# Kernel tuning notes

Measured on AMD Instinct MI355X. Metric: run time of the kernel, lower is better.

## Reference

```python
import jax, jax.numpy as jnp
import numpy as np

FEAT, HW, C, M, U, B = 2048, 14, 20, 64, 128, 4


def _grid_sample_one(img, grid):
    # img: [M, H, W]; grid: [H, W, 2] normalized coords (x, y), align_corners=True, zero padding
    H, W = img.shape[-2], img.shape[-1]
    gx = (grid[..., 0] + 1.0) * 0.5 * (W - 1)
    gy = (grid[..., 1] + 1.0) * 0.5 * (H - 1)
    x0 = jnp.floor(gx).astype(jnp.int32); x1 = x0 + 1
    y0 = jnp.floor(gy).astype(jnp.int32); y1 = y0 + 1

    def gather(yi, xi):
        valid = (yi >= 0) & (yi < H) & (xi >= 0) & (xi < W)
        yc = jnp.clip(yi, 0, H - 1); xc = jnp.clip(xi, 0, W - 1)
        return img[:, yc, xc] * valid.astype(img.dtype)  # [M, H, W]

    w00 = (x1 - gx) * (y1 - gy); w01 = (gx - x0) * (y1 - gy)
    w10 = (x1 - gx) * (gy - y0); w11 = (gx - x0) * (gy - y0)
    return (gather(y0, x0) * w00 + gather(y0, x1) * w01 +
            gather(y1, x0) * w10 + gather(y1, x1) * w11)


def setup_inputs() -> dict:
    key = jax.random.key(0)
    ks = jax.random.split(key, 5)
    x = jax.random.normal(ks[0], (B, FEAT, HW, HW), jnp.float32)
    W_parcel = jax.random.normal(ks[1], (C, M, FEAT), jnp.float32) * 0.02
    W_stn = jax.random.normal(ks[2], (C, 6, M * (HW // 2) ** 2), jnp.float32) * 1e-3
    b_stn = jnp.tile(jnp.array([1.0, 0.0, 0.0, 0.0, 1.0, 0.0], jnp.float32), (C, 1))
    Wg = jax.random.normal(ks[3], (C, C - 1, U, 2 * M), jnp.float32) * 0.02
    w_phi = jax.random.normal(ks[4], (1, U), jnp.float32) * 0.05
    b_phi = jnp.zeros((1,), jnp.float32)
    return {"x": x, "W_parcel": W_parcel, "W_stn": W_stn, "b_stn": b_stn,
            "Wg": Wg, "w_phi": w_phi, "b_phi": b_phi}


def reference(x, W_parcel, W_stn, b_stn, Wg, w_phi, b_phi):
    b, _, H, W = x.shape
    # per-class 1x1 conv parcels: [B, C, M, H, W]
    x_tmp = jnp.einsum('bfhw,cmf->bcmhw', x, W_parcel)
    # relu + 2x2 maxpool -> [B, C, M, 7, 7]
    pooled = jax.nn.relu(x_tmp).reshape(b, C, M, H // 2, 2, W // 2, 2).max(axis=(4, 6))
    flat = pooled.reshape(b, C, M * (H // 2) * (W // 2))
    theta = (jnp.einsum('bck,cjk->bcj', flat, W_stn) + b_stn).reshape(b, C, 2, 3)
    # affine grid (align_corners=True): base[h, w] = [x_norm, y_norm, 1]
    xs = jnp.linspace(-1.0, 1.0, W); ys = jnp.linspace(-1.0, 1.0, H)
    base = jnp.stack(jnp.broadcast_arrays(xs[None, :], ys[:, None], jnp.ones((H, W))), -1)
    grid = jnp.einsum('bcij,hwj->bchwi', theta, base)  # [B, C, H, W, 2]
    # STN sampling of the pre-relu parcel maps
    x_obj = jax.vmap(jax.vmap(_grid_sample_one))(x_tmp, grid)  # [B, C, M, H, W]
    # pairwise relation: relu(Wa[i,j] x_obj[i] + Wb[i,j] x_obj[j]) summed over j != i
    jidx = jnp.asarray(np.array([[k for k in range(C) if k != c] for c in range(C)]))
    Wa, Wb = Wg[..., :M], Wg[..., M:]
    A = jnp.einsum('ckum,bcmhw->bckuhw', Wa, x_obj)
    Bp = jnp.einsum('ckum,bckmhw->bckuhw', Wb, x_obj[:, jidx])
    rel = jax.nn.relu(A + Bp).sum(axis=2)          # [B, C, U, H, W]
    rel_mean = rel.mean(axis=(-2, -1))             # [B, C, U]  (adaptive avg pool 1x1)
    out = jnp.einsum('bcu,ou->bco', rel_mean, w_phi)[..., 0] + b_phi  # [B, C]
    return out
```

## Files before the change

### kernel.cpp

```cpp
#include <hip/hip_runtime.h>

#define FEAT 2048
#define HWD 14
#define NPIX 196
#define C_CLS 20
#define M_DIM 64
#define U_DIM 128
#define B_SZ 4
#define K_REL 19
#define NPOOL 49

typedef __attribute__((ext_vector_type(8))) short bf16x8s;
typedef __attribute__((ext_vector_type(8))) unsigned short ushort8v;
typedef __attribute__((ext_vector_type(4))) float f32x4;
typedef __attribute__((ext_vector_type(4))) unsigned int uint4v;

__device__ inline unsigned short f2bf(float f) {
    unsigned u = __builtin_bit_cast(unsigned, f);
    unsigned r = (u + 0x7FFF + ((u >> 16) & 1)) >> 16;
    return (unsigned short)r;
}

__device__ inline bf16x8s cvt8(const float* __restrict__ p) {
    float4 lo = *(const float4*)p;
    float4 hi = *(const float4*)(p + 4);
    bf16x8s r;
    r[0] = (short)f2bf(lo.x); r[1] = (short)f2bf(lo.y);
    r[2] = (short)f2bf(lo.z); r[3] = (short)f2bf(lo.w);
    r[4] = (short)f2bf(hi.x); r[5] = (short)f2bf(hi.y);
    r[6] = (short)f2bf(hi.z); r[7] = (short)f2bf(hi.w);
    return r;
}

__global__ __launch_bounds__(256) void prep_kernel(
        const float* __restrict__ x, const float* __restrict__ Wg,
        const float* __restrict__ Wp,
        unsigned short* __restrict__ xts, unsigned short* __restrict__ Wgb,
        unsigned short* __restrict__ Awp) {
    __shared__ unsigned short T[64][210];
    const int blk = blockIdx.x;
    const int tid = threadIdx.x;
    if (blk < 128) {
        const int b = blk >> 5;
        const int s = blk & 31;
        const float* xb = x + ((size_t)b * FEAT + s * 64) * NPIX;
        for (int i = tid; i < 64 * NPIX; i += 256) {
            int kk = i / NPIX, hw = i - kk * NPIX;
            T[kk][hw] = f2bf(xb[(size_t)kk * NPIX + hw]);
        }
        __syncthreads();
        unsigned short* ob = xts + ((size_t)(b * 32 + s)) * 1664 * 8;
        for (int i = tid; i < 1664; i += 256) {
            int ch = i / 208, row = i - ch * 208;
            ushort8v o;
#pragma unroll
            for (int j = 0; j < 8; j++)
                o[j] = (row < NPIX) ? T[ch * 8 + j][row] : (unsigned short)0;
            *(ushort8v*)(ob + (size_t)i * 8) = o;
        }
    } else {
        const int lane = tid & 63;
        int gw = (blk - 128) * 4 + (tid >> 6);
        for (int r = gw; r < 5120; r += 896 * 4) {
            int c = r >> 8;
            int rem = r & 255;
            int s = rem >> 3, fi = rem & 7;
            int rt = fi >> 1, f = fi & 1;
            int m = rt * 16 + (lane & 15);
            int k = s * 64 + f * 32 + (lane >> 4) * 8;
            bf16x8s v = cvt8(Wp + ((size_t)(c * M_DIM + m)) * FEAT + k);
            *(bf16x8s*)(Awp + ((size_t)r * 64 + lane) * 8) = v;
        }
        const int NWG4 = C_CLS * K_REL * U_DIM * 2 * M_DIM / 4;
        for (int gi = (blk - 128) * 256 + tid; gi < NWG4; gi += 896 * 256) {
            float4 v = *(const float4*)(Wg + (size_t)gi * 4);
            ushort4 o;
            o.x = f2bf(v.x); o.y = f2bf(v.y); o.z = f2bf(v.z); o.w = f2bf(v.w);
            *(ushort4*)(Wgb + (size_t)gi * 4) = o;
        }
    }
}

#define KP2 72
__global__ __launch_bounds__(512) void fused_kernel(
        const unsigned short* __restrict__ xts,
        const unsigned short* __restrict__ Awp,
        const float* __restrict__ Wstn,
        const float* __restrict__ bstn,
        unsigned short* __restrict__ x_objT) {
    __shared__ __align__(16) char smem[78336];
    unsigned short* Xs0 = (unsigned short*)smem;
    unsigned short* Xs1 = (unsigned short*)(smem + 29952);
    float* xs     = (float*)smem;
    float* pooled = (float*)(smem + 53504);
    float* red    = (float*)(smem + 66048);

    const int c = blockIdx.x, b = blockIdx.y;
    const int tid = threadIdx.x;
    const int lane = tid & 63, wv = tid >> 6;
    const int l15 = lane & 15, lq = lane >> 4;
    const int rg = wv & 1;
    const int cg = wv >> 1;
    const int cs = (cg == 0) ? 0 : (3 * cg + 1);
    const int nct = (cg == 0) ? 4 : 3;

    const unsigned short* xsrc = xts + (size_t)b * 32 * 1664 * 8;
    const unsigned short* asrc = Awp + (size_t)c * 256 * 64 * 8;

    int ldsoff[4]; size_t goff[4]; bool gvalid[4];
#pragma unroll
    for (int it = 0; it < 4; it++) {
        int i = it * 512 + tid;
        gvalid[it] = (i < 1664);
        int ii = gvalid[it] ? i : 0;
        int ch = ii / 208, row = ii - ch * 208;
        ldsoff[it] = row * KP2 + ch * 8;
        goff[it] = (size_t)ii * 8;
    }

    uint4v SA[4], SB[4];
    auto g_issue = [&](int s, uint4v (&S)[4]) {
        const unsigned short* src = xsrc + (size_t)s * 1664 * 8;
#pragma unroll
        for (int it = 0; it < 4; it++)
            if (gvalid[it]) S[it] = *(const uint4v*)(src + goff[it]);
    };
    auto l_write = [&](unsigned short* buf, uint4v (&S)[4]) {
#pragma unroll
        for (int it = 0; it < 4; it++)
            if (gvalid[it]) *(uint4v*)(buf + ldsoff[it]) = S[it];
    };

    bf16x8s AF[2][2], AFn[2][2];
    auto aload = [&](int s, bf16x8s (&A)[2][2]) {
#pragma unroll
        for (int rt2 = 0; rt2 < 2; rt2++)
#pragma unroll
            for (int f = 0; f < 2; f++) {
                int fi = (rg * 2 + rt2) * 2 + f;
                A[rt2][f] = *(const bf16x8s*)(asrc + (((size_t)s * 8 + fi) * 64 + lane) * 8);
            }
    };

    f32x4 acc[2][4];
#pragma unroll
    for (int rt2 = 0; rt2 < 2; rt2++)
#pragma unroll
        for (int q = 0; q < 4; q++) acc[rt2][q] = (f32x4){0.f, 0.f, 0.f, 0.f};

    auto compute = [&](const unsigned short* Xb, bf16x8s (&A)[2][2]) {
#pragma unroll
        for (int q = 0; q < 4; q++) {
            if (q < nct) {
                int tt = cs + q;
#pragma unroll
                for (int f = 0; f < 2; f++) {
                    bf16x8s Bf = *(const bf16x8s*)(&Xb[(tt * 16 + l15) * KP2 + f * 32 + lq * 8]);
                    acc[0][q] = __builtin_amdgcn_mfma_f32_16x16x32_bf16(A[0][f], Bf, acc[0][q], 0, 0, 0);
                    acc[1][q] = __builtin_amdgcn_mfma_f32_16x16x32_bf16(A[1][f], Bf, acc[1][q], 0, 0, 0);
                }
            }
        }
    };

    g_issue(0, SA);
    g_issue(1, SB);
    aload(0, AF);
    l_write(Xs0, SA);
    __syncthreads();

    for (int sp = 0; sp < 16; sp++) {
        aload(2 * sp + 1, AFn);
        compute(Xs0, AF);
        if (sp < 15) g_issue(2 * sp + 2, SA);
        l_write(Xs1, SB);
        __syncthreads();
        if (sp < 15) aload(2 * sp + 2, AF);
        compute(Xs1, AFn);
        if (sp < 15) {
            g_issue(2 * sp + 3, SB);
            l_write(Xs0, SA);
        }
        __syncthreads();
    }

#pragma unroll
    for (int q = 0; q < 4; q++) {
        if (q < nct) {
            int tt = cs + q;
#pragma unroll
            for (int rt2 = 0; rt2 < 2; rt2++) {
                int row0 = (rg * 2 + rt2) * 16 + lq * 4;
#pragma unroll
                for (int r = 0; r < 4; r++)
                    xs[(row0 + r) * 209 + tt * 16 + l15] = acc[rt2][q][r];
            }
        }
    }
    __syncthreads();

    for (int i = tid; i < 3136; i += 512) {
        int m = i / NPOOL, p = i - m * NPOOL;
        int ph = p / 7, pw = p - ph * 7;
        const float* bp = &xs[m * 209 + ph * 2 * HWD + pw * 2];
        float v = fmaxf(fmaxf(bp[0], bp[1]), fmaxf(bp[HWD], bp[HWD + 1]));
        pooled[i] = fmaxf(v, 0.f);
    }
    __syncthreads();

    float sj[6] = {0, 0, 0, 0, 0, 0};
#pragma unroll
    for (int it = 0; it < 7; it++) {
        int kk = tid + it * 512;
        if (kk < 3136) {
            float f = pooled[kk];
#pragma unroll
            for (int j = 0; j < 6; j++)
                sj[j] += f * Wstn[((size_t)c * 6 + j) * 3136 + kk];
        }
    }
#pragma unroll
    for (int j = 0; j < 6; j++) red[j * 512 + tid] = sj[j];
    __syncthreads();
    for (int off = 256; off > 0; off >>= 1) {
        if (tid < off) {
#pragma unroll
            for (int j = 0; j < 6; j++)
                red[j * 512 + tid] += red[j * 512 + tid + off];
        }
        __syncthreads();
    }
    float th[6];
#pragma unroll
    for (int j = 0; j < 6; j++) th[j] = red[j * 512] + bstn[c * 6 + j];

    const int m = tid & 63;
    const int hwg = tid >> 6;
    unsigned short* ob = x_objT + ((size_t)(b * C_CLS + c) * NPIX) * 64 + m;
    const float* xrow = &xs[m * 209];
    for (int it = 0; it < 25; it++) {
        int hw = hwg + it * 8;
        if (hw >= NPIX) break;
        int h = hw / HWD, w = hw - h * HWD;
        float fx = -1.f + w * (2.f / 13.f);
        float fy = -1.f + h * (2.f / 13.f);
        float gxn = th[0] * fx + th[1] * fy + th[2];
        float gyn = th[3] * fx + th[4] * fy + th[5];
        float gx = (gxn + 1.f) * 0.5f * (HWD - 1);
        float gy = (gyn + 1.f) * 0.5f * (HWD - 1);
        float x0f = floorf(gx), y0f = floorf(gy);
        int x0 = (int)x0f, y0 = (int)y0f;
        int x1 = x0 + 1, y1 = y0 + 1;
        auto gat = [&](int yi, int xi) -> float {
            bool v = (yi >= 0) & (yi < HWD) & (xi >= 0) & (xi < HWD);
            int yc = min(max(yi, 0), HWD - 1);
            int xc = min(max(xi, 0), HWD - 1);
            return v ? xrow[yc * HWD + xc] : 0.f;
        };
        float xw1 = (float)x1 - gx, xw0 = gx - (float)x0;
        float yw1 = (float)y1 - gy, yw0 = gy - (float)y0;
        float val = gat(y0, x0) * xw1 * yw1 + gat(y0, x1) * xw0 * yw1 +
                    gat(y1, x0) * xw1 * yw0 + gat(y1, x1) * xw0 * yw0;
        ob[(size_t)hw * 64] = f2bf(val);
    }
}

#define MP 136
__global__ __launch_bounds__(256) void relation_mfma_kernel(
        const unsigned short* __restrict__ x_objT,
        const unsigned short* __restrict__ Wgb,
        float* __restrict__ partial) {
    __shared__ unsigned short Xs[208 * MP];
    const int k = blockIdx.x;
    const int c = blockIdx.y;
    const int b = blockIdx.z;
    const int kj = (k < c) ? k : k + 1;
    const int tid = threadIdx.x;
    const int lane = tid & 63;
    const int wv = tid >> 6;
    const int l15 = lane & 15;
    const int lq = lane >> 4;

    bf16x8s AF[2][4];
    const unsigned short* wgb = Wgb + (((size_t)c * K_REL + k) * U_DIM) * (2 * M_DIM);
#pragma unroll
    for (int ut = 0; ut < 2; ut++) {
        int u = wv * 32 + ut * 16 + l15;
#pragma unroll
        for (int ks = 0; ks < 4; ks++)
            AF[ut][ks] = *(const bf16x8s*)(wgb + (size_t)u * 128 + ks * 32 + lq * 8);
    }

    const unsigned short* xc = x_objT + ((size_t)(b * C_CLS + c)) * NPIX * 64;
    const unsigned short* xk = x_objT + ((size_t)(b * C_CLS + kj)) * NPIX * 64;
#pragma unroll
    for (int it = 0; it < 13; it++) {
        int i = tid + it * 256;
        int hw = i >> 4, ch = i & 15;
        uint4v v = {0, 0, 0, 0};
        if (hw < NPIX) {
            const unsigned short* src = (ch < 8 ? xc : xk) + (size_t)hw * 64 + (ch & 7) * 8;
            v = *(const uint4v*)src;
        }
        *(uint4v*)(&Xs[hw * MP + ch * 8]) = v;
    }
    __syncthreads();

    float csum[2][4];
#pragma unroll
    for (int ut = 0; ut < 2; ut++)
#pragma unroll
        for (int r = 0; r < 4; r++) csum[ut][r] = 0.f;

    for (int t = 0; t < 13; t++) {
        bf16x8s BF[4];
#pragma unroll
        for (int ks = 0; ks < 4; ks++)
            BF[ks] = *(const bf16x8s*)(&Xs[(t * 16 + l15) * MP + ks * 32 + lq * 8]);
        f32x4 acc0 = {0.f, 0.f, 0.f, 0.f}, acc1 = {0.f, 0.f, 0.f, 0.f};
#pragma unroll
        for (int ks = 0; ks < 4; ks++) {
            acc0 = __builtin_amdgcn_mfma_f32_16x16x32_bf16(AF[0][ks], BF[ks], acc0, 0, 0, 0);
            acc1 = __builtin_amdgcn_mfma_f32_16x16x32_bf16(AF[1][ks], BF[ks], acc1, 0, 0, 0);
        }
#pragma unroll
        for (int r = 0; r < 4; r++) {
            csum[0][r] += fmaxf(acc0[r], 0.f);
            csum[1][r] += fmaxf(acc1[r], 0.f);
        }
    }
#pragma unroll
    for (int mask = 1; mask < 16; mask <<= 1) {
#pragma unroll
        for (int ut = 0; ut < 2; ut++)
#pragma unroll
            for (int r = 0; r < 4; r++)
                csum[ut][r] += __shfl_xor(csum[ut][r], mask, 64);
    }
    if (l15 == 0) {
        float* pp = partial + (((size_t)b * C_CLS + c) * K_REL + k) * U_DIM;
#pragma unroll
        for (int ut = 0; ut < 2; ut++)
#pragma unroll
            for (int r = 0; r < 4; r++)
                pp[wv * 32 + ut * 16 + lq * 4 + r] = csum[ut][r];
    }
}

__global__ __launch_bounds__(128) void final_kernel(
        const float* __restrict__ partial, const float* __restrict__ wphi,
        const float* __restrict__ bphi, float* __restrict__ out) {
    int bc = blockIdx.x;
    int u = threadIdx.x;
    float s = 0.f;
    for (int k = 0; k < K_REL; k++)
        s += partial[((size_t)bc * K_REL + k) * U_DIM + u];
    s *= wphi[u];
    __shared__ float red[128];
    red[u] = s;
    __syncthreads();
    for (int off = 64; off > 0; off >>= 1) {
        if (u < off) red[u] += red[u + off];
        __syncthreads();
    }
    if (u == 0) out[bc] = red[0] / (float)NPIX + bphi[0];
}

extern "C" void kernel_launch(void* const* d_in, const int* in_sizes, int n_in,
                              void* d_out, int out_size, void* d_ws, size_t ws_size,
                              hipStream_t stream) {
    const float* x    = (const float*)d_in[0];
    const float* Wp   = (const float*)d_in[1];
    const float* Wstn = (const float*)d_in[2];
    const float* bstn = (const float*)d_in[3];
    const float* Wg   = (const float*)d_in[4];
    const float* wphi = (const float*)d_in[5];
    const float* bphi = (const float*)d_in[6];
    float* out = (float*)d_out;
    char* wsb = (char*)d_ws;

    unsigned short* xts    = (unsigned short*)(wsb);
    unsigned short* Wgb    = (unsigned short*)(wsb + 3407872);
    unsigned short* Awp    = (unsigned short*)(wsb + 15859712);
    unsigned short* x_objT = (unsigned short*)(wsb + 21102592);
    float* partial         = (float*)(wsb + 23109632);

    prep_kernel<<<1024, 256, 0, stream>>>(x, Wg, Wp, xts, Wgb, Awp);
    fused_kernel<<<dim3(C_CLS, B_SZ), 512, 0, stream>>>(xts, Awp, Wstn, bstn, x_objT);
    relation_mfma_kernel<<<dim3(K_REL, C_CLS, B_SZ), 256, 0, stream>>>(x_objT, Wgb, partial);
    final_kernel<<<80, 128, 0, stream>>>(partial, wphi, bphi, out);
}
```

Baseline: 74.69 us.

## Load MFMA operands directly from global memory, dropping LDS staging and barriers

The parcel GEMM stage no longer stages x tiles through double-buffered shared memory with block-wide barriers. Each wave now loads its own B fragments straight from global memory into registers and holds all four A row tiles, with a register double-buffer across K steps. Work is repartitioned so each wave owns one or two column tiles across all 64 rows. This removes LDS writes, LDS reads and 32 syncthreads per block, at the cost of more redundant global/L2 reads of A (every wave loads all A fragments) and uneven work across waves (5 waves with 2 tiles, 3 with 1).

```diff
diff --git a/kernel.cpp b/kernel.cpp
--- a/kernel.cpp
+++ b/kernel.cpp
@@ -81,7 +81,6 @@
     }
 }
 
-#define KP2 72
 __global__ __launch_bounds__(512) void fused_kernel(
         const unsigned short* __restrict__ xts,
         const unsigned short* __restrict__ Awp,
@@ -89,8 +88,6 @@
         const float* __restrict__ bstn,
         unsigned short* __restrict__ x_objT) {
     __shared__ __align__(16) char smem[78336];
-    unsigned short* Xs0 = (unsigned short*)smem;
-    unsigned short* Xs1 = (unsigned short*)(smem + 29952);
     float* xs     = (float*)smem;
     float* pooled = (float*)(smem + 53504);
     float* red    = (float*)(smem + 66048);
@@ -99,102 +96,67 @@
     const int tid = threadIdx.x;
     const int lane = tid & 63, wv = tid >> 6;
     const int l15 = lane & 15, lq = lane >> 4;
-    const int rg = wv & 1;
-    const int cg = wv >> 1;
-    const int cs = (cg == 0) ? 0 : (3 * cg + 1);
-    const int nct = (cg == 0) ? 4 : 3;
+    const int t0 = (wv < 5) ? 2 * wv : 10 + (wv - 5);
+    const int nt = (wv < 5) ? 2 : 1;
 
     const unsigned short* xsrc = xts + (size_t)b * 32 * 1664 * 8;
     const unsigned short* asrc = Awp + (size_t)c * 256 * 64 * 8;
 
-    int ldsoff[4]; size_t goff[4]; bool gvalid[4];
-#pragma unroll
-    for (int it = 0; it < 4; it++) {
-        int i = it * 512 + tid;
-        gvalid[it] = (i < 1664);
-        int ii = gvalid[it] ? i : 0;
-        int ch = ii / 208, row = ii - ch * 208;
-        ldsoff[it] = row * KP2 + ch * 8;
-        goff[it] = (size_t)ii * 8;
-    }
-
-    uint4v SA[4], SB[4];
-    auto g_issue = [&](int s, uint4v (&S)[4]) {
-        const unsigned short* src = xsrc + (size_t)s * 1664 * 8;
-#pragma unroll
-        for (int it = 0; it < 4; it++)
-            if (gvalid[it]) S[it] = *(const uint4v*)(src + goff[it]);
+    bf16x8s A0[8], A1[8], B0[4], B1[4];
+    auto aload = [&](int s, bf16x8s (&A)[8]) {
+#pragma unroll
+        for (int fi = 0; fi < 8; fi++)
+            A[fi] = *(const bf16x8s*)(asrc + (((size_t)s * 8 + fi) * 64 + lane) * 8);
     };
-    auto l_write = [&](unsigned short* buf, uint4v (&S)[4]) {
-#pragma unroll
-        for (int it = 0; it < 4; it++)
-            if (gvalid[it]) *(uint4v*)(buf + ldsoff[it]) = S[it];
+    auto bload = [&](int s, bf16x8s (&B)[4]) {
+#pragma unroll
+        for (int q = 0; q < 2; q++) {
+            if (q < nt) {
+#pragma unroll
+                for (int f = 0; f < 2; f++)
+                    B[q * 2 + f] = *(const bf16x8s*)(xsrc +
+                        ((size_t)s * 1664 + (f * 4 + lq) * 208 + (t0 + q) * 16 + l15) * 8);
+            }
+        }
     };
 
-    bf16x8s AF[2][2], AFn[2][2];
-    auto aload = [&](int s, bf16x8s (&A)[2][2]) {
-#pragma unroll
-        for (int rt2 = 0; rt2 < 2; rt2++)
-#pragma unroll
-            for (int f = 0; f < 2; f++) {
-                int fi = (rg * 2 + rt2) * 2 + f;
-                A[rt2][f] = *(const bf16x8s*)(asrc + (((size_t)s * 8 + fi) * 64 + lane) * 8);
+    f32x4 acc[2][4];
+#pragma unroll
+    for (int q = 0; q < 2; q++)
+#pragma unroll
+        for (int rt = 0; rt < 4; rt++) acc[q][rt] = (f32x4){0.f, 0.f, 0.f, 0.f};
+
+    auto compute = [&](bf16x8s (&A)[8], bf16x8s (&B)[4]) {
+#pragma unroll
+        for (int q = 0; q < 2; q++) {
+            if (q < nt) {
+#pragma unroll
+                for (int rt = 0; rt < 4; rt++)
+#pragma unroll
+                    for (int f = 0; f < 2; f++)
+                        acc[q][rt] = __builtin_amdgcn_mfma_f32_16x16x32_bf16(
+                            A[rt * 2 + f], B[q * 2 + f], acc[q][rt], 0, 0, 0);
             }
+        }
     };
 
-    f32x4 acc[2][4];
-#pragma unroll
-    for (int rt2 = 0; rt2 < 2; rt2++)
-#pragma unroll
-        for (int q = 0; q < 4; q++) acc[rt2][q] = (f32x4){0.f, 0.f, 0.f, 0.f};
-
-    auto compute = [&](const unsigned short* Xb, bf16x8s (&A)[2][2]) {
-#pragma unroll
-        for (int q = 0; q < 4; q++) {
-            if (q < nct) {
-                int tt = cs + q;
-#pragma unroll
-                for (int f = 0; f < 2; f++) {
-                    bf16x8s Bf = *(const bf16x8s*)(&Xb[(tt * 16 + l15) * KP2 + f * 32 + lq * 8]);
-                    acc[0][q] = __builtin_amdgcn_mfma_f32_16x16x32_bf16(A[0][f], Bf, acc[0][q], 0, 0, 0);
-                    acc[1][q] = __builtin_amdgcn_mfma_f32_16x16x32_bf16(A[1][f], Bf, acc[1][q], 0, 0, 0);
-                }
-            }
-        }
-    };
-
-    g_issue(0, SA);
-    g_issue(1, SB);
-    aload(0, AF);
-    l_write(Xs0, SA);
-    __syncthreads();
-
+    aload(0, A0); bload(0, B0);
     for (int sp = 0; sp < 16; sp++) {
-        aload(2 * sp + 1, AFn);
-        compute(Xs0, AF);
-        if (sp < 15) g_issue(2 * sp + 2, SA);
-        l_write(Xs1, SB);
-        __syncthreads();
-        if (sp < 15) aload(2 * sp + 2, AF);
-        compute(Xs1, AFn);
-        if (sp < 15) {
-            g_issue(2 * sp + 3, SB);
-            l_write(Xs0, SA);
-        }
-        __syncthreads();
-    }
-
-#pragma unroll
-    for (int q = 0; q < 4; q++) {
-        if (q < nct) {
-            int tt = cs + q;
-#pragma unroll
-            for (int rt2 = 0; rt2 < 2; rt2++) {
-                int row0 = (rg * 2 + rt2) * 16 + lq * 4;
+        aload(2 * sp + 1, A1); bload(2 * sp + 1, B1);
+        compute(A0, B0);
+        if (sp < 15) { aload(2 * sp + 2, A0); bload(2 * sp + 2, B0); }
+        compute(A1, B1);
+    }
+
+#pragma unroll
+    for (int q = 0; q < 2; q++) {
+        if (q < nt) {
+            int tt = t0 + q;
+#pragma unroll
+            for (int rt = 0; rt < 4; rt++)
 #pragma unroll
                 for (int r = 0; r < 4; r++)
-                    xs[(row0 + r) * 209 + tt * 16 + l15] = acc[rt2][q][r];
-            }
+                    xs[(rt * 16 + lq * 4 + r) * 209 + tt * 16 + l15] = acc[q][rt][r];
         }
     }
     __syncthreads();
```

After: 77.28 us. 3.5% more time.
